# Kernel optimization log

Hardware: AMD Instinct MI355X
Metric: run time of the kernel (lower is better)

## Reference

```python
import jax, jax.numpy as jnp
import numpy as np

B, N, D, H, K, MSL = 16, 512, 512, 8, 16, 512
HD = D // H
EPS = 1e-5


def _ln(x, g, b):
    m = jnp.mean(x, axis=-1, keepdims=True)
    v = jnp.mean((x - m) ** 2, axis=-1, keepdims=True)
    return (x - m) * jax.lax.rsqrt(v + EPS) * g + b


def setup_inputs() -> dict:
    key = jax.random.key(0)
    ks = jax.random.split(key, 12)
    s = 0.02
    d = {
        'x': jax.random.normal(ks[0], (B, N, D), jnp.float32),
        'wq': jax.random.normal(ks[1], (D, D), jnp.float32) * s,
        'bq': jnp.zeros((D,), jnp.float32),
        'wk': jax.random.normal(ks[2], (D, D), jnp.float32) * s,
        'bk': jnp.zeros((D,), jnp.float32),
        'wv': jax.random.normal(ks[3], (D, D), jnp.float32) * s,
        'bv': jnp.zeros((D,), jnp.float32),
        'wo': jax.random.normal(ks[4], (D, D), jnp.float32) * s,
        'bo': jnp.zeros((D,), jnp.float32),
        'g1': jnp.ones((D,), jnp.float32),
        'be1': jnp.zeros((D,), jnp.float32),
        'g2': jnp.ones((D,), jnp.float32),
        'be2': jnp.zeros((D,), jnp.float32),
        'w1': jax.random.normal(ks[5], (D, 4 * D), jnp.float32) * s,
        'bf1': jnp.zeros((4 * D,), jnp.float32),
        'w2': jax.random.normal(ks[6], (4 * D, D), jnp.float32) * s,
        'bf2': jnp.zeros((D,), jnp.float32),
        'rel_emb': jax.random.normal(ks[7], (2 * MSL - 1, H), jnp.float32) * s,
    }
    return d


def reference(x, wq, bq, wk, bk, wv, bv, wo, bo, g1, be1, g2, be2, w1, bf1, w2, bf2, rel_emb):
    # Pre-norm attention (dropout = identity, eval mode)
    xn = _ln(x, g1, be1)
    Q = (xn @ wq + bq).reshape(B, N, H, HD)
    Kh = (xn @ wk + bk).reshape(B, N, H, HD)
    V = (xn @ wv + bv).reshape(B, N, H, HD)
    scale = HD ** -0.5
    logits = jnp.einsum('bnhd,bmhd->bhnm', Q, Kh) * scale  # (B,H,N,N)
    # relative temporal bias
    pos = jnp.arange(N)
    drel = pos[None, :] - pos[:, None] + (MSL - 1)  # (N,N)
    bias = rel_emb[drel]  # (N,N,H)
    logits = logits + jnp.transpose(bias, (2, 0, 1))[None]
    # top-k sparsification + softmax over surviving entries only
    vals, idx = jax.lax.top_k(logits, K)  # (B,H,N,K)
    attn_k = jax.nn.softmax(vals, axis=-1)  # softmax over -inf-masked row == softmax over top-k
    # scatter probabilities back into dense (B,H,N,N) rows
    rows = jnp.zeros((B * H * N, N), logits.dtype)
    attn = jax.vmap(lambda r, i, v: r.at[i].set(v))(
        rows, idx.reshape(-1, K), attn_k.reshape(-1, K)
    ).reshape(B, H, N, N)
    out = jnp.einsum('bhnm,bmhd->bnhd', attn, V).reshape(B, N, D)
    out = out @ wo + bo
    x = x + out
    # feed-forward (GELU exact, matching torch default)
    xn2 = _ln(x, g2, be2)
    ff = jax.nn.gelu(xn2 @ w1 + bf1, approximate=False) @ w2 + bf2
    return x + ff
```

## Files before the change

### kernel.cpp

```cpp
#include <hip/hip_runtime.h>
#include <hip/hip_bf16.h>

#define BB 16
#define NN 512
#define DD 512
#define HH 8
#define HD 64
#define MM (BB*NN)
#define DFF 2048

typedef __attribute__((ext_vector_type(8))) short bf16x8;
typedef __attribute__((ext_vector_type(4))) float fx4;

static __device__ __forceinline__ unsigned short f2bf(float f) {
  unsigned u = __float_as_uint(f);
  u += 0x7FFFu + ((u >> 16) & 1u);
  return (unsigned short)(u >> 16);
}
static __device__ __forceinline__ float bf2f(unsigned short s) {
  return __uint_as_float(((unsigned)s) << 16);
}

static __device__ __forceinline__ void load_lds16(const unsigned short* g, unsigned short* l) {
  __builtin_amdgcn_global_load_lds(
      (const __attribute__((address_space(1))) void*)g,
      (__attribute__((address_space(3))) void*)l, 16, 0, 0);
}

static __device__ __forceinline__ unsigned dpp_sum16(unsigned v) {
  v += (unsigned)__builtin_amdgcn_update_dpp(0, (int)v, 0xB1, 0xF, 0xF, false);
  v += (unsigned)__builtin_amdgcn_update_dpp(0, (int)v, 0x4E, 0xF, 0xF, false);
  v += (unsigned)__builtin_amdgcn_update_dpp(0, (int)v, 0x124, 0xF, 0xF, false);
  v += (unsigned)__builtin_amdgcn_update_dpp(0, (int)v, 0x128, 0xF, 0xF, false);
  return v;
}
static __device__ __forceinline__ unsigned dpp_min16(unsigned v) {
  unsigned o;
  o = (unsigned)__builtin_amdgcn_update_dpp(0, (int)v, 0xB1, 0xF, 0xF, false);  v = o < v ? o : v;
  o = (unsigned)__builtin_amdgcn_update_dpp(0, (int)v, 0x4E, 0xF, 0xF, false);  v = o < v ? o : v;
  o = (unsigned)__builtin_amdgcn_update_dpp(0, (int)v, 0x124, 0xF, 0xF, false); v = o < v ? o : v;
  o = (unsigned)__builtin_amdgcn_update_dpp(0, (int)v, 0x128, 0xF, 0xF, false); v = o < v ? o : v;
  return v;
}
static __device__ __forceinline__ unsigned dpp_max16(unsigned v) {
  unsigned o;
  o = (unsigned)__builtin_amdgcn_update_dpp(0, (int)v, 0xB1, 0xF, 0xF, false);  v = o > v ? o : v;
  o = (unsigned)__builtin_amdgcn_update_dpp(0, (int)v, 0x4E, 0xF, 0xF, false);  v = o > v ? o : v;
  o = (unsigned)__builtin_amdgcn_update_dpp(0, (int)v, 0x124, 0xF, 0xF, false); v = o > v ? o : v;
  o = (unsigned)__builtin_amdgcn_update_dpp(0, (int)v, 0x128, 0xF, 0xF, false); v = o > v ? o : v;
  return v;
}

__global__ void transpose_all(const float* __restrict__ wq, const float* __restrict__ wk,
                              const float* __restrict__ wv, const float* __restrict__ wo,
                              const float* __restrict__ w1, const float* __restrict__ w2,
                              unsigned short* __restrict__ wqkvT, unsigned short* __restrict__ woT,
                              unsigned short* __restrict__ w1T, unsigned short* __restrict__ w2T) {
  __shared__ float tl[32][33];
  int id = blockIdx.x;
  const float* src; unsigned short* dst; int K, N, bx, by;
  if (id < 1024) {
    int m = id >> 8, tt = id & 255;
    src = (m == 0) ? wq : (m == 1) ? wk : (m == 2) ? wv : wo;
    dst = (m == 3) ? woT : wqkvT + m * 512 * 512;
    K = 512; N = 512; bx = tt & 15; by = tt >> 4;
  } else if (id < 2048) {
    int tt = id - 1024;
    src = w1; dst = w1T; K = 512; N = 2048; bx = tt & 63; by = tt >> 6;
  } else {
    int tt = id - 2048;
    src = w2; dst = w2T; K = 2048; N = 512; bx = tt & 15; by = tt >> 4;
  }
  int tx = threadIdx.x, ty = threadIdx.y;
  int x0 = bx * 32, y0 = by * 32;
  #pragma unroll
  for (int i = 0; i < 4; i++)
    tl[ty + i*8][tx] = src[(size_t)(y0 + ty + i*8) * N + x0 + tx];
  __syncthreads();
  #pragma unroll
  for (int i = 0; i < 4; i++)
    dst[(size_t)(x0 + ty + i*8) * K + y0 + tx] = f2bf(tl[tx][ty + i*8]);
}

__global__ void concat_bias(const float* __restrict__ bq, const float* __restrict__ bk,
                            const float* __restrict__ bv, float* __restrict__ o) {
  int t = blockIdx.x * 256 + threadIdx.x;
  if (t < 512) o[t] = bq[t];
  else if (t < 1024) o[t] = bk[t - 512];
  else if (t < 1536) o[t] = bv[t - 1024];
}

__global__ __launch_bounds__(256) void ln_kernel(const float* __restrict__ X,
                                                 const float* __restrict__ g,
                                                 const float* __restrict__ be,
                                                 unsigned short* __restrict__ O) {
  int w = threadIdx.x >> 6, l = threadIdx.x & 63;
  size_t row = (size_t)blockIdx.x * 4 + w;
  const float* xr = X + row * 512;
  fx4 a = *(const fx4*)(xr + l*4);
  fx4 c = *(const fx4*)(xr + 256 + l*4);
  float s = a[0]+a[1]+a[2]+a[3] + c[0]+c[1]+c[2]+c[3];
  float q = a[0]*a[0]+a[1]*a[1]+a[2]*a[2]+a[3]*a[3]
          + c[0]*c[0]+c[1]*c[1]+c[2]*c[2]+c[3]*c[3];
  #pragma unroll
  for (int s2 = 1; s2 < 64; s2 <<= 1) { s += __shfl_xor(s, s2); q += __shfl_xor(q, s2); }
  float mean = s * (1.0f/512.0f);
  float var  = q * (1.0f/512.0f) - mean*mean;
  float rs = rsqrtf(var + 1e-5f);
  fx4 ga = *(const fx4*)(g + l*4);
  fx4 gc = *(const fx4*)(g + 256 + l*4);
  fx4 ba = *(const fx4*)(be + l*4);
  fx4 bc = *(const fx4*)(be + 256 + l*4);
  ushort4 o1, o2;
  o1.x = f2bf((a[0]-mean)*rs*ga[0] + ba[0]);
  o1.y = f2bf((a[1]-mean)*rs*ga[1] + ba[1]);
  o1.z = f2bf((a[2]-mean)*rs*ga[2] + ba[2]);
  o1.w = f2bf((a[3]-mean)*rs*ga[3] + ba[3]);
  o2.x = f2bf((c[0]-mean)*rs*gc[0] + bc[0]);
  o2.y = f2bf((c[1]-mean)*rs*gc[1] + bc[1]);
  o2.z = f2bf((c[2]-mean)*rs*gc[2] + bc[2]);
  o2.w = f2bf((c[3]-mean)*rs*gc[3] + bc[3]);
  *(ushort4*)(O + row*512 + l*4) = o1;
  *(ushort4*)(O + row*512 + 256 + l*4) = o2;
}

template<int MODE, int TN>
__global__ __launch_bounds__(256) void gemm_kernel(
    const unsigned short* __restrict__ A,
    const unsigned short* __restrict__ Bm,
    const float* __restrict__ bias,
    const float* resid,
    void* C,
    int M, int N, int K) {
  constexpr int MI  = (TN == 128) ? 2 : 1;
  constexpr int BW  = (TN == 128) ? 32 : 16;
  constexpr int NBI = (TN == 128) ? 4 : 2;
  __shared__ unsigned short As[64*64];
  __shared__ unsigned short Bs[TN*64];
  int m0 = blockIdx.y * 64, n0 = blockIdx.x * TN;
  int t = threadIdx.x;
  int w = t >> 6, l = t & 63;
  int wm = (TN == 128) ? (w >> 1) : w;
  int wn = (TN == 128) ? (w & 1) : 0;
  int lid = l & 15, quad = l >> 4;
  int lrow = l >> 3, lch = (l & 7) ^ lrow;

  const unsigned short* gA = A  + (size_t)(m0 + w*16 + lrow)*K + lch*8;
  const unsigned short* gB = Bm + (size_t)(n0 + w*BW + lrow)*K + lch*8;
  unsigned short* lA0 = As + (w*16    )*64;
  unsigned short* lA1 = As + (w*16 + 8)*64;
  unsigned short* lB[NBI];
  #pragma unroll
  for (int i = 0; i < NBI; i++) lB[i] = Bs + (w*BW + i*8)*64;

  fx4 acc[MI][4];
  #pragma unroll
  for (int i = 0; i < MI; i++)
    #pragma unroll
    for (int j = 0; j < 4; j++) acc[i][j] = (fx4){0.f,0.f,0.f,0.f};

  int xA = (lid & 7) * 8;

  for (int k0 = 0; k0 < K; k0 += 64) {
    load_lds16(gA,       lA0);
    load_lds16(gA + 8*K, lA1);
    #pragma unroll
    for (int i = 0; i < NBI; i++) load_lds16(gB + (size_t)(i*8)*K, lB[i]);
    gA += 64; gB += 64;
    __syncthreads();
    #pragma unroll
    for (int s = 0; s < 2; s++) {
      int cbase = (s*4 + quad) * 8;
      bf16x8 af[MI], bf[4];
      #pragma unroll
      for (int i = 0; i < MI; i++) {
        int ra = wm*(MI*16) + i*16 + lid;
        af[i] = *(const bf16x8*)(As + ra*64 + (cbase ^ xA));
      }
      #pragma unroll
      for (int j = 0; j < 4; j++) {
        int rb = wn*64 + j*16 + lid;
        bf[j] = *(const bf16x8*)(Bs + rb*64 + (cbase ^ xA));
      }
      #pragma unroll
      for (int i = 0; i < MI; i++)
        #pragma unroll
        for (int j = 0; j < 4; j++)
          acc[i][j] = __builtin_amdgcn_mfma_f32_16x16x32_bf16(af[i], bf[j], acc[i][j], 0, 0, 0);
    }
    __syncthreads();
  }

  #pragma unroll
  for (int i = 0; i < MI; i++) {
    #pragma unroll
    for (int j = 0; j < 4; j++) {
      int col = n0 + wn*64 + j*16 + lid;
      float bv = bias[col];
      #pragma unroll
      for (int r = 0; r < 4; r++) {
        int row = m0 + wm*(MI*16) + i*16 + quad*4 + r;
        float v = acc[i][j][r] + bv;
        if (MODE == 0) {
          if (col < 512) v *= 0.125f;
          ((unsigned short*)C)[(size_t)row*N + col] = f2bf(v);
        } else if (MODE == 1 || MODE == 3) {
          v += resid[(size_t)row*N + col];
          ((float*)C)[(size_t)row*N + col] = v;
        } else {
          float gl = 0.5f * v * (1.0f + erff(v * 0.70710678118654752f));
          ((unsigned short*)C)[(size_t)row*N + col] = f2bf(gl);
        }
      }
    }
  }
}

__global__ __launch_bounds__(256) void attn_kernel(
    const unsigned short* __restrict__ QKV,
    const float* __restrict__ rel_emb,
    unsigned short* __restrict__ Aout) {
  __shared__ float smem[6144];
  unsigned short* Ks = (unsigned short*)smem;
  float* bias_s = smem + 4096;
  float* pr = smem + 5120;
  int blk = blockIdx.x;
  int q0 = (blk & 7) << 6;
  int bh = blk >> 3;
  int b = bh >> 3, h = bh & 7;
  int t = threadIdx.x;
  int w = t >> 6, l = t & 63;
  int lid = l & 15, quad = l >> 4;

  for (int i = t; i < 1023; i += 256) bias_s[i] = rel_emb[i*8 + h];

  int qn = q0 + w*16 + lid;
  const unsigned short* qp = QKV + ((size_t)(b*512 + qn))*1536 + h*64 + quad*8;
  bf16x8 qf0 = *(const bf16x8*)qp;
  bf16x8 qf1 = *(const bf16x8*)(qp + 32);

  fx4 acc[32];
  #pragma unroll
  for (int i = 0; i < 32; i++) acc[i] = (fx4){0.f,0.f,0.f,0.f};

  int xk = lid & 7;
  #pragma unroll
  for (int chunk = 0; chunk < 4; chunk++) {
    __syncthreads();
    #pragma unroll
    for (int i = 0; i < 4; i++) {
      int c = t + i*256;
      int row = c >> 3, ch = c & 7;
      uint4 d = *(const uint4*)(QKV + ((size_t)(b*512 + chunk*128 + row))*1536 + 512 + h*64 + ch*8);
      *(uint4*)(Ks + row*64 + ((ch ^ (row & 7))*8)) = d;
    }
    __syncthreads();
    #pragma unroll
    for (int kt = 0; kt < 8; kt++) {
      const unsigned short* kp = Ks + (kt*16 + lid)*64;
      bf16x8 kb0 = *(const bf16x8*)(kp + ((quad    ) ^ xk)*8);
      bf16x8 kb1 = *(const bf16x8*)(kp + ((quad + 4) ^ xk)*8);
      int ai = chunk*8 + kt;
      acc[ai] = __builtin_amdgcn_mfma_f32_16x16x32_bf16(qf0, kb0, acc[ai], 0, 0, 0);
      acc[ai] = __builtin_amdgcn_mfma_f32_16x16x32_bf16(qf1, kb1, acc[ai], 0, 0, 0);
    }
  }

  int nb = q0 + w*16 + quad*4;
  #pragma unroll
  for (int kt = 0; kt < 32; kt++) {
    int m = kt*16 + lid;
    int bidx = m - nb + 511;
    #pragma unroll
    for (int r = 0; r < 4; r++) {
      float v = acc[kt][r] + bias_s[bidx - r];
      unsigned mu = __float_as_uint(v);
      mu = (mu & 0x80000000u) ? ~mu : (mu | 0x80000000u);
      acc[kt][r] = __uint_as_float((mu & 0xFFFFFE00u) | (unsigned)(511 - m));
    }
  }

  unsigned mx0=0, mx1=0, mx2=0, mx3=0;
  #pragma unroll
  for (int kt = 0; kt < 32; kt++) {
    unsigned u0 = __float_as_uint(acc[kt][0]); mx0 = u0 > mx0 ? u0 : mx0;
    unsigned u1 = __float_as_uint(acc[kt][1]); mx1 = u1 > mx1 ? u1 : mx1;
    unsigned u2 = __float_as_uint(acc[kt][2]); mx2 = u2 > mx2 ? u2 : mx2;
    unsigned u3 = __float_as_uint(acc[kt][3]); mx3 = u3 > mx3 ? u3 : mx3;
  }
  unsigned mn0 = dpp_min16(mx0), mn1 = dpp_min16(mx1);
  unsigned mn2 = dpp_min16(mx2), mn3 = dpp_min16(mx3);
  mx0 = dpp_max16(mx0); mx1 = dpp_max16(mx1);
  mx2 = dpp_max16(mx2); mx3 = dpp_max16(mx3);
  unsigned lo0 = mn0 - (mn0 ? 1u : 0u), hi0 = mx0;
  unsigned lo1 = mn1 - (mn1 ? 1u : 0u), hi1 = mx1;
  unsigned lo2 = mn2 - (mn2 ? 1u : 0u), hi2 = mx2;
  unsigned lo3 = mn3 - (mn3 ? 1u : 0u), hi3 = mx3;

  unsigned th0=0, th1=0, th2=0, th3=0;
  unsigned done = 0;
  #pragma unroll 1
  for (int it = 0; it < 34; ++it) {
    unsigned d_;
    d_ = hi0-lo0; unsigned mid0 = lo0 + (d_>>1) + (d_&1u);
    d_ = hi1-lo1; unsigned mid1 = lo1 + (d_>>1) + (d_&1u);
    d_ = hi2-lo2; unsigned mid2 = lo2 + (d_>>1) + (d_&1u);
    d_ = hi3-lo3; unsigned mid3 = lo3 + (d_>>1) + (d_&1u);
    unsigned c0=0, c1=0, c2=0, c3=0;
    #pragma unroll
    for (int kt = 0; kt < 32; kt++) {
      c0 += (__float_as_uint(acc[kt][0]) >= mid0);
      c1 += (__float_as_uint(acc[kt][1]) >= mid1);
      c2 += (__float_as_uint(acc[kt][2]) >= mid2);
      c3 += (__float_as_uint(acc[kt][3]) >= mid3);
    }
    unsigned p01 = dpp_sum16(c0 | (c1 << 16));
    unsigned p23 = dpp_sum16(c2 | (c3 << 16));
    unsigned C0 = p01 & 0xFFFFu, C1 = p01 >> 16;
    unsigned C2 = p23 & 0xFFFFu, C3 = p23 >> 16;
    { bool f = !(done & 1u); bool e = f && (C0 == 16u);
      th0 = e ? mid0 : th0; done |= e ? 1u : 0u;
      lo0 = (f && C0 > 16u) ? mid0 : lo0; hi0 = (f && C0 < 16u) ? mid0 : hi0; }
    { bool f = !(done & 2u); bool e = f && (C1 == 16u);
      th1 = e ? mid1 : th1; done |= e ? 2u : 0u;
      lo1 = (f && C1 > 16u) ? mid1 : lo1; hi1 = (f && C1 < 16u) ? mid1 : hi1; }
    { bool f = !(done & 4u); bool e = f && (C2 == 16u);
      th2 = e ? mid2 : th2; done |= e ? 4u : 0u;
      lo2 = (f && C2 > 16u) ? mid2 : lo2; hi2 = (f && C2 < 16u) ? mid2 : hi2; }
    { bool f = !(done & 8u); bool e = f && (C3 == 16u);
      th3 = e ? mid3 : th3; done |= e ? 8u : 0u;
      lo3 = (f && C3 > 16u) ? mid3 : lo3; hi3 = (f && C3 < 16u) ? mid3 : hi3; }
    if (__all((int)(done == 15u))) break;
  }

  unsigned below = (1u << lid) - 1u;
  #pragma unroll
  for (int r = 0; r < 4; r++) {
    float* prE = pr + (r & 1)*512 + w*128 + quad*32;
    int*   prM = (int*)prE + 16;
    unsigned thr = (r==0) ? th0 : (r==1) ? th1 : (r==2) ? th2 : th3;
    int base = 0;
    #pragma unroll
    for (int kt = 0; kt < 32; kt++) {
      unsigned u = __float_as_uint(acc[kt][r]);
      bool sel = u >= thr;
      unsigned long long bm = __ballot(sel);
      unsigned gm = (unsigned)(bm >> (quad*16)) & 0xFFFFu;
      if (sel) {
        int slot = base + __popc(gm & below);
        unsigned vu = u & 0xFFFFFE00u;
        vu = (vu & 0x80000000u) ? (vu & 0x7FFFFFFFu) : ~vu;
        float e = exp2f(__uint_as_float(vu) * 1.44269504f);
        if (slot < 16) { prE[slot] = e; prM[slot] = 511 - (int)(u & 0x1FFu); }
      }
      base += __popc(gm);
    }
    __threadfence_block();
    int n = nb + r;
    float o0=0.f, o1=0.f, o2=0.f, o3=0.f, es=0.f;
    #pragma unroll
    for (int k2 = 0; k2 < 16; k2++) {
      float e = prE[k2];
      int m = prM[k2];
      const unsigned short* vp = QKV + ((size_t)(b*512 + m))*1536 + 1024 + h*64 + lid*4;
      ushort4 v4 = *(const ushort4*)vp;
      es += e;
      o0 += e * bf2f(v4.x); o1 += e * bf2f(v4.y);
      o2 += e * bf2f(v4.z); o3 += e * bf2f(v4.w);
    }
    float inv = 1.0f / es;
    ushort4 ov;
    ov.x = f2bf(o0*inv); ov.y = f2bf(o1*inv);
    ov.z = f2bf(o2*inv); ov.w = f2bf(o3*inv);
    *(ushort4*)(Aout + ((size_t)(b*512 + n))*512 + h*64 + lid*4) = ov;
  }
}

extern "C" void kernel_launch(void* const* d_in, const int* in_sizes, int n_in,
                              void* d_out, int out_size, void* d_ws, size_t ws_size,
                              hipStream_t stream) {
  const float* x   = (const float*)d_in[0];
  const float* wq  = (const float*)d_in[1];
  const float* bq  = (const float*)d_in[2];
  const float* wk  = (const float*)d_in[3];
  const float* bk  = (const float*)d_in[4];
  const float* wv  = (const float*)d_in[5];
  const float* bv  = (const float*)d_in[6];
  const float* wo  = (const float*)d_in[7];
  const float* bo  = (const float*)d_in[8];
  const float* g1  = (const float*)d_in[9];
  const float* be1 = (const float*)d_in[10];
  const float* g2  = (const float*)d_in[11];
  const float* be2 = (const float*)d_in[12];
  const float* w1  = (const float*)d_in[13];
  const float* bf1 = (const float*)d_in[14];
  const float* w2  = (const float*)d_in[15];
  const float* bf2 = (const float*)d_in[16];
  const float* rel = (const float*)d_in[17];

  char* p = (char*)d_ws;
  size_t off = 0;
  auto alloc = [&](size_t bytes) {
    size_t cur = off;
    off += (bytes + 255) & ~(size_t)255;
    return (void*)(p + cur);
  };
  unsigned short* wqkvT = (unsigned short*)alloc((size_t)1536*512*2);
  unsigned short* woT   = (unsigned short*)alloc((size_t)512*512*2);
  unsigned short* w1T   = (unsigned short*)alloc((size_t)2048*512*2);
  unsigned short* w2T   = (unsigned short*)alloc((size_t)512*2048*2);
  float*          bqkv  = (float*)alloc(1536*4);
  unsigned short* R1    = (unsigned short*)alloc((size_t)MM*512*2);
  unsigned short* R2    = (unsigned short*)alloc((size_t)MM*2048*2);

  unsigned short* xn1  = R1;
  unsigned short* aout = R1;
  unsigned short* xn2  = R1;
  unsigned short* qkvb = R2;
  unsigned short* hbuf = R2;
  float*          x2   = (float*)d_out;
  (void)ws_size; (void)in_sizes; (void)n_in; (void)out_size;

  transpose_all<<<3072, dim3(32, 8), 0, stream>>>(wq, wk, wv, wo, w1, w2,
                                                  wqkvT, woT, w1T, w2T);
  concat_bias<<<6, 256, 0, stream>>>(bq, bk, bv, bqkv);

  ln_kernel<<<2048, 256, 0, stream>>>(x, g1, be1, xn1);
  gemm_kernel<0,128><<<dim3(12, 128), 256, 0, stream>>>(xn1, wqkvT, bqkv, nullptr, qkvb, MM, 1536, 512);
  attn_kernel<<<1024, 256, 0, stream>>>(qkvb, rel, aout);
  gemm_kernel<1,64><<<dim3(8, 128), 256, 0, stream>>>(aout, woT, bo, x, x2, MM, 512, 512);
  ln_kernel<<<2048, 256, 0, stream>>>(x2, g2, be2, xn2);
  gemm_kernel<2,128><<<dim3(16, 128), 256, 0, stream>>>(xn2, w1T, bf1, nullptr, hbuf, MM, 2048, 512);
  gemm_kernel<3,64><<<dim3(8, 128), 256, 0, stream>>>(hbuf, w2T, bf2, x2, (float*)d_out, MM, 512, 2048);
}
```

Baseline: 385.6 us.

## Double-buffer GEMM LDS tiles to overlap global loads with MFMA compute

The GEMM kernel now keeps two LDS buffers for the A and B tiles. It prefetches the next K-slice with global_load_lds while MFMAs run on the current slice. This removes the end-of-iteration barrier and hides global-to-LDS latency behind compute. The cost is double the LDS footprint per block, which can lower occupancy.

```diff
diff --git a/kernel.cpp b/kernel.cpp
--- a/kernel.cpp
+++ b/kernel.cpp
@@ -135,8 +135,8 @@
   constexpr int MI  = (TN == 128) ? 2 : 1;
   constexpr int BW  = (TN == 128) ? 32 : 16;
   constexpr int NBI = (TN == 128) ? 4 : 2;
-  __shared__ unsigned short As[64*64];
-  __shared__ unsigned short Bs[TN*64];
+  __shared__ unsigned short As[2*64*64];
+  __shared__ unsigned short Bs[2*TN*64];
   int m0 = blockIdx.y * 64, n0 = blockIdx.x * TN;
   int t = threadIdx.x;
   int w = t >> 6, l = t & 63;
@@ -147,11 +147,8 @@
 
   const unsigned short* gA = A  + (size_t)(m0 + w*16 + lrow)*K + lch*8;
   const unsigned short* gB = Bm + (size_t)(n0 + w*BW + lrow)*K + lch*8;
-  unsigned short* lA0 = As + (w*16    )*64;
-  unsigned short* lA1 = As + (w*16 + 8)*64;
-  unsigned short* lB[NBI];
-  #pragma unroll
-  for (int i = 0; i < NBI; i++) lB[i] = Bs + (w*BW + i*8)*64;
+  int aoff0 = (w*16    )*64;
+  int aoff1 = (w*16 + 8)*64;
 
   fx4 acc[MI][4];
   #pragma unroll
@@ -161,13 +158,26 @@
 
   int xA = (lid & 7) * 8;
 
+  load_lds16(gA,       As + aoff0);
+  load_lds16(gA + 8*K, As + aoff1);
+  #pragma unroll
+  for (int i = 0; i < NBI; i++) load_lds16(gB + (size_t)(i*8)*K, Bs + (w*BW + i*8)*64);
+
   for (int k0 = 0; k0 < K; k0 += 64) {
-    load_lds16(gA,       lA0);
-    load_lds16(gA + 8*K, lA1);
-    #pragma unroll
-    for (int i = 0; i < NBI; i++) load_lds16(gB + (size_t)(i*8)*K, lB[i]);
-    gA += 64; gB += 64;
+    int cur = (k0 >> 6) & 1;
+    unsigned short* Ac = As + cur*4096;
+    unsigned short* Bc = Bs + cur*TN*64;
     __syncthreads();
+    if (k0 + 64 < K) {
+      unsigned short* An = As + (cur^1)*4096;
+      unsigned short* Bn = Bs + (cur^1)*TN*64;
+      load_lds16(gA + 64,       An + aoff0);
+      load_lds16(gA + 64 + 8*K, An + aoff1);
+      #pragma unroll
+      for (int i = 0; i < NBI; i++)
+        load_lds16(gB + 64 + (size_t)(i*8)*K, Bn + (w*BW + i*8)*64);
+      gA += 64; gB += 64;
+    }
     #pragma unroll
     for (int s = 0; s < 2; s++) {
       int cbase = (s*4 + quad) * 8;
@@ -175,12 +185,12 @@
       #pragma unroll
       for (int i = 0; i < MI; i++) {
         int ra = wm*(MI*16) + i*16 + lid;
-        af[i] = *(const bf16x8*)(As + ra*64 + (cbase ^ xA));
+        af[i] = *(const bf16x8*)(Ac + ra*64 + (cbase ^ xA));
       }
       #pragma unroll
       for (int j = 0; j < 4; j++) {
         int rb = wn*64 + j*16 + lid;
-        bf[j] = *(const bf16x8*)(Bs + rb*64 + (cbase ^ xA));
+        bf[j] = *(const bf16x8*)(Bc + rb*64 + (cbase ^ xA));
       }
       #pragma unroll
       for (int i = 0; i < MI; i++)
@@ -188,7 +198,6 @@
         for (int j = 0; j < 4; j++)
           acc[i][j] = __builtin_amdgcn_mfma_f32_16x16x32_bf16(af[i], bf[j], acc[i][j], 0, 0, 0);
     }
-    __syncthreads();
   }
 
   #pragma unroll
```

New measurement: 385.0 us. Within noise of the previous version (-0.1%).
